# Kernel optimization log

Hardware: AMD Instinct MI355X
Metric: run time of the kernel (lower is better)

Reference implementation:

```python
import jax, jax.numpy as jnp
import numpy as np

TEMPERATURE = 1.0

def _rope_cos_sin(T, D):
    # inv_freq over even indices 0..D step 2 -> D//2 freqs
    inv_freq = 1.0 / (10000.0 ** (jnp.arange(0, D, 2, dtype=jnp.float32) / D))
    t = jnp.arange(T, dtype=jnp.float32)
    freqs = jnp.einsum('i,j->ij', t, inv_freq)          # [T, D//2]
    emb = jnp.concatenate([freqs, freqs], axis=-1)      # [T, D]
    return jnp.cos(emb), jnp.sin(emb)                   # each [T, D]

def _apply_rope(x, cos, sin):
    # x: [B,H,T,D]; cos/sin: [T,D] broadcast over B,H
    D = x.shape[-1]
    half = D // 2
    x1, x2 = x[..., :half], x[..., half:2 * half]
    c = cos[None, None, :, :half]
    s = sin[None, None, :, :half]
    rot = jnp.concatenate([x1 * c - x2 * s, x1 * s + x2 * c], axis=-1)
    if D > 2 * half:
        rot = jnp.concatenate([rot, x[..., 2 * half:]], axis=-1)
    return rot

def setup_inputs() -> dict:
    key = jax.random.key(0)
    kq, kk, kv = jax.random.split(key, 3)
    B, H, T, D = 2, 16, 2048, 64
    return {
        'q': jax.random.normal(kq, (B, H, T, D), dtype=jnp.float32),
        'k': jax.random.normal(kk, (B, H, T, D), dtype=jnp.float32),
        'v': jax.random.normal(kv, (B, H, T, D), dtype=jnp.float32),
    }

def reference(q, k, v):
    B, H, T, D = q.shape
    cos, sin = _rope_cos_sin(T, D)
    qr = _apply_rope(q, cos, sin)
    kr = _apply_rope(k, cos, sin)
    scale = jnp.sqrt(jnp.float32(D)) * TEMPERATURE
    scores = jnp.einsum('bhtd,bhsd->bhts', qr, kr) / scale  # [B,H,T,T]
    # original subtracts row max then softmax; identical to stable softmax
    attn = jax.nn.softmax(scores, axis=-1)
    out = jnp.einsum('bhts,bhsd->bhtd', attn, v)
    return out, attn
```

## Files before the change

kernel.cpp:

```cpp
#include <hip/hip_runtime.h>
#include <hip/hip_bf16.h>
#include <math.h>


#define T_SEQ  2048
#define D_HEAD 64
#define BH_N   32
#define NCH    32
#define OUT_ELEMS (BH_N * T_SEQ * D_HEAD)

typedef __attribute__((ext_vector_type(8))) short bf16x8;
typedef __attribute__((ext_vector_type(4))) float f32x4;

__device__ __forceinline__ unsigned short f2bf(float x) {
    __hip_bfloat16 h = __float2bfloat16(x);
    return *reinterpret_cast<unsigned short*>(&h);
}

__device__ __forceinline__ int swz(int o) { return o ^ (((o >> 7) & 7) << 4); }

__global__ void rope_table_kernel(float* __restrict__ ctab, float* __restrict__ stab) {
    int i = blockIdx.x * blockDim.x + threadIdx.x;
    if (i >= T_SEQ * 32) return;
    int t = i >> 5;
    int j = i & 31;
    float invf = powf(10000.0f, -(float)j / 32.0f);
    float a = (float)t * invf;
    ctab[i] = cosf(a);
    stab[i] = sinf(a);
}

__global__ __launch_bounds__(256)
void ropebf16_kernel(const float* __restrict__ X, const float* __restrict__ ctab,
                     const float* __restrict__ stab, unsigned short* __restrict__ H,
                     float scale)
{
    const int r  = blockIdx.x * 16 + (threadIdx.x >> 4);
    const int c4 = threadIdx.x & 15;
    const int t  = r & (T_SEQ - 1);
    const float4* xr = (const float4*)(X + (size_t)r * 64);
    float4 a = xr[c4];
    float4 b = xr[c4 ^ 8];
    float4 c = ((const float4*)(ctab + t * 32))[c4 & 7];
    float4 s = ((const float4*)(stab + t * 32))[c4 & 7];
    float4 ro;
    if (c4 < 8) {
        ro.x = a.x * c.x - b.x * s.x; ro.y = a.y * c.y - b.y * s.y;
        ro.z = a.z * c.z - b.z * s.z; ro.w = a.w * c.w - b.w * s.w;
    } else {
        ro.x = a.x * c.x + b.x * s.x; ro.y = a.y * c.y + b.y * s.y;
        ro.z = a.z * c.z + b.z * s.z; ro.w = a.w * c.w + b.w * s.w;
    }
    ushort4 h;
    h.x = f2bf(ro.x * scale); h.y = f2bf(ro.y * scale);
    h.z = f2bf(ro.z * scale); h.w = f2bf(ro.w * scale);
    *(ushort4*)(H + (size_t)r * 64 + c4 * 4) = h;
}

__global__ __launch_bounds__(256)
void vtbf16_kernel(const float* __restrict__ V, unsigned short* __restrict__ Vt)
{
    __shared__ float tile[64][65];
    const int bh = blockIdx.y;
    const int tt = blockIdx.x;
    const float* vg = V + ((size_t)bh * T_SEQ + tt * 64) * 64;
    #pragma unroll
    for (int i = 0; i < 4; ++i) {
        const int row = (threadIdx.x >> 4) + i * 16;
        const int c4  = threadIdx.x & 15;
        float4 a = *(const float4*)(vg + (size_t)row * 64 + c4 * 4);
        tile[row][c4 * 4 + 0] = a.x; tile[row][c4 * 4 + 1] = a.y;
        tile[row][c4 * 4 + 2] = a.z; tile[row][c4 * 4 + 3] = a.w;
    }
    __syncthreads();
    #pragma unroll
    for (int i = 0; i < 4; ++i) {
        const int d   = (threadIdx.x >> 4) + i * 16;
        const int tc4 = threadIdx.x & 15;
        ushort4 h;
        h.x = f2bf(tile[tc4 * 4 + 0][d]);
        h.y = f2bf(tile[tc4 * 4 + 1][d]);
        h.z = f2bf(tile[tc4 * 4 + 2][d]);
        h.w = f2bf(tile[tc4 * 4 + 3][d]);
        *(ushort4*)(Vt + ((size_t)bh * 64 + d) * T_SEQ + tt * 64 + tc4 * 4) = h;
    }
}

__global__ __launch_bounds__(256, 4)
void attn_mfma_kernel(const unsigned short* __restrict__ Qb,
                      const unsigned short* __restrict__ Kb,
                      const unsigned short* __restrict__ Vt,
                      float* __restrict__ out, float* __restrict__ attn)
{
    __shared__ __align__(16) unsigned short kbuf[3][64][64];
    __shared__ __align__(16) unsigned short pbuf[4][16][72];

    const int tid  = threadIdx.x;
    const int lane = tid & 63;
    const int w    = tid >> 6;
    const int lrow = lane & 15;
    const int lgrp = lane >> 4;

    const int lid = blockIdx.x;
    const int vid = (lid & 7) * 128 + (lid >> 3);
    const int bh  = vid >> 5;
    const int m   = vid & 31;
    const int t0  = m * 64 + w * 16;

    const size_t base = (size_t)bh * T_SEQ * D_HEAD;
    const char* kgb = (const char*)(Kb + base);
    const unsigned short* vgb = Vt + (size_t)bh * 64 * T_SEQ;

    bf16x8 qf0, qf1;
    {
        const unsigned short* qp = Qb + base + (size_t)(t0 + lrow) * 64 + lgrp * 8;
        qf0 = *(const bf16x8*)(qp);
        qf1 = *(const bf16x8*)(qp + 32);
    }

    const int so0 = w * 1024 + lane * 16;
    const int so1 = so0 + 4096;
    const int sq0 = swz(so0);
    const int sq1 = swz(so1);
    char* klds = (char*)&kbuf[0][0][0];
    char* plds = (char*)&pbuf[w][0][0];

#define STAGE_K(b, cc) do { \
    __builtin_amdgcn_global_load_lds((const unsigned int*)(kgb + (size_t)(cc) * 8192 + sq0), \
        (unsigned int*)(klds + (b) * 8192 + w * 1024), 16, 0, 0); \
    __builtin_amdgcn_global_load_lds((const unsigned int*)(kgb + (size_t)(cc) * 8192 + sq1), \
        (unsigned int*)(klds + (b) * 8192 + 4096 + w * 1024), 16, 0, 0); \
} while (0)

    float rpa0 = 0.f, rpa1 = 0.f, rpa2 = 0.f, rpa3 = 0.f;
    STAGE_K(0, 0);
    STAGE_K(1, 1);
    for (int cc = 0; cc < NCH; ++cc) {
        if (cc < NCH - 1) { asm volatile("s_waitcnt vmcnt(2)" ::: "memory"); }
        else              { asm volatile("s_waitcnt vmcnt(0)" ::: "memory"); }
        __builtin_amdgcn_s_barrier();
        if (cc + 2 < NCH) STAGE_K((cc + 2) % 3, cc + 2);
        __builtin_amdgcn_sched_barrier(0);
        const char* kb = klds + (cc % 3) * 8192;
        #pragma unroll
        for (int nt = 0; nt < 4; ++nt) {
            const int o = (nt * 16 + lrow) * 128 + lgrp * 16;
            bf16x8 a0 = *(const bf16x8*)(kb + swz(o));
            bf16x8 a1 = *(const bf16x8*)(kb + swz(o + 64));
            f32x4 acc = (f32x4){0.f, 0.f, 0.f, 0.f};
            acc = __builtin_amdgcn_mfma_f32_16x16x32_bf16(a0, qf0, acc, 0, 0, 0);
            acc = __builtin_amdgcn_mfma_f32_16x16x32_bf16(a1, qf1, acc, 0, 0, 0);
            rpa0 += __builtin_amdgcn_exp2f(acc[0]);
            rpa1 += __builtin_amdgcn_exp2f(acc[1]);
            rpa2 += __builtin_amdgcn_exp2f(acc[2]);
            rpa3 += __builtin_amdgcn_exp2f(acc[3]);
        }
    }
    float rp = (rpa0 + rpa1) + (rpa2 + rpa3);
    rp += __shfl_xor(rp, 16, 64);
    rp += __shfl_xor(rp, 32, 64);
    const float inv = 1.0f / rp;

    __builtin_amdgcn_sched_barrier(0);
    __builtin_amdgcn_s_barrier();

    f32x4 o4[4];
    #pragma unroll
    for (int nd = 0; nd < 4; ++nd) o4[nd] = (f32x4){0.f, 0.f, 0.f, 0.f};

    float* arow = attn + (size_t)bh * T_SEQ * T_SEQ + (size_t)(t0 + lrow) * T_SEQ + lgrp * 4;

    STAGE_K(0, 0);
    STAGE_K(1, 1);
    bf16x8 vf[8];
    #pragma unroll
    for (int nd = 0; nd < 4; ++nd)
        #pragma unroll
        for (int ks = 0; ks < 2; ++ks)
            vf[nd * 2 + ks] = *(const bf16x8*)(vgb + (size_t)(nd * 16 + lrow) * T_SEQ
                                               + ks * 32 + lgrp * 8);
    asm volatile("s_waitcnt vmcnt(10)" ::: "memory");

    for (int cc = 0; cc < NCH; ++cc) {
        __builtin_amdgcn_s_barrier();
        __builtin_amdgcn_sched_barrier(0);

        const char* kb = klds + (cc % 3) * 8192;
        f32x4 s4[4];
        #pragma unroll
        for (int nt = 0; nt < 4; ++nt) {
            const int o = (nt * 16 + lrow) * 128 + lgrp * 16;
            bf16x8 a0 = *(const bf16x8*)(kb + swz(o));
            bf16x8 a1 = *(const bf16x8*)(kb + swz(o + 64));
            f32x4 acc = (f32x4){0.f, 0.f, 0.f, 0.f};
            acc = __builtin_amdgcn_mfma_f32_16x16x32_bf16(a0, qf0, acc, 0, 0, 0);
            acc = __builtin_amdgcn_mfma_f32_16x16x32_bf16(a1, qf1, acc, 0, 0, 0);
            s4[nt] = acc;
        }
        #pragma unroll
        for (int nt = 0; nt < 4; ++nt) {
            s4[nt][0] = __builtin_amdgcn_exp2f(s4[nt][0]) * inv;
            s4[nt][1] = __builtin_amdgcn_exp2f(s4[nt][1]) * inv;
            s4[nt][2] = __builtin_amdgcn_exp2f(s4[nt][2]) * inv;
            s4[nt][3] = __builtin_amdgcn_exp2f(s4[nt][3]) * inv;
        }
        #pragma unroll
        for (int nt = 0; nt < 4; ++nt) {
            ushort4 p4;
            p4.x = f2bf(s4[nt][0]); p4.y = f2bf(s4[nt][1]);
            p4.z = f2bf(s4[nt][2]); p4.w = f2bf(s4[nt][3]);
            *(ushort4*)(plds + lrow * 144 + nt * 32 + lgrp * 8) = p4;
        }
        asm volatile("s_waitcnt lgkmcnt(0)" ::: "memory");
        __builtin_amdgcn_sched_barrier(0);
        #pragma unroll
        for (int ks = 0; ks < 2; ++ks) {
            bf16x8 pa = *(const bf16x8*)(plds + lrow * 144 + ks * 64 + lgrp * 16);
            #pragma unroll
            for (int nd = 0; nd < 4; ++nd)
                o4[nd] = __builtin_amdgcn_mfma_f32_16x16x32_bf16(pa, vf[nd * 2 + ks], o4[nd], 0, 0, 0);
        }
        __builtin_amdgcn_sched_barrier(0);
        if (cc + 1 < NCH) {
            #pragma unroll
            for (int nd = 0; nd < 4; ++nd)
                #pragma unroll
                for (int ks = 0; ks < 2; ++ks)
                    vf[nd * 2 + ks] = *(const bf16x8*)(vgb + (size_t)(nd * 16 + lrow) * T_SEQ
                                                       + (cc + 1) * 64 + ks * 32 + lgrp * 8);
        }
        if (cc + 2 < NCH) STAGE_K((cc + 2) % 3, cc + 2);
        __builtin_amdgcn_sched_barrier(0);
        #pragma unroll
        for (int nt = 0; nt < 4; ++nt)
            __builtin_nontemporal_store(s4[nt], (f32x4*)(arow + cc * 64 + nt * 16));
        __builtin_amdgcn_sched_barrier(0);
        if (cc < NCH - 2)      { asm volatile("s_waitcnt vmcnt(18)" ::: "memory"); }
        else if (cc < NCH - 1) { asm volatile("s_waitcnt vmcnt(16)" ::: "memory"); }
    }

    #pragma unroll
    for (int nd = 0; nd < 4; ++nd)
        #pragma unroll
        for (int j = 0; j < 4; ++j)
            __builtin_nontemporal_store(o4[nd][j],
                out + base + (size_t)(t0 + lgrp * 4 + j) * D_HEAD + nd * 16 + lrow);

#undef STAGE_K
}

extern "C" void kernel_launch(void* const* d_in, const int* in_sizes, int n_in,
                              void* d_out, int out_size, void* d_ws, size_t ws_size,
                              hipStream_t stream) {
    const float* q = (const float*)d_in[0];
    const float* k = (const float*)d_in[1];
    const float* v = (const float*)d_in[2];
    float* out  = (float*)d_out;
    float* attn = out + (size_t)OUT_ELEMS;

    float* ctab = (float*)d_ws;
    float* stab = ctab + T_SEQ * 32;
    unsigned short* wsu = (unsigned short*)(stab + T_SEQ * 32);
    const size_t NE = (size_t)BH_N * T_SEQ * D_HEAD;
    unsigned short* Qb = wsu + 0 * NE;
    unsigned short* Kb = wsu + 1 * NE;
    unsigned short* Vt = wsu + 2 * NE;

    const float QSCALE = 0.18033688011112042f;

    rope_table_kernel<<<dim3((T_SEQ * 32 + 255) / 256), dim3(256), 0, stream>>>(ctab, stab);
    ropebf16_kernel<<<dim3(BH_N * T_SEQ / 16), dim3(256), 0, stream>>>(q, ctab, stab, Qb, QSCALE);
    ropebf16_kernel<<<dim3(BH_N * T_SEQ / 16), dim3(256), 0, stream>>>(k, ctab, stab, Kb, 1.0f);
    vtbf16_kernel<<<dim3(T_SEQ / 64, BH_N), dim3(256), 0, stream>>>(v, Vt);
    attn_mfma_kernel<<<dim3(BH_N * T_SEQ / 64), dim3(256), 0, stream>>>(Qb, Kb, Vt, out, attn);
}
```

Baseline: 206.8 us.

## Stage fp32 probabilities in LDS for coalesced attn stores; merge Q/K rope launches

Softmax probabilities are now written to a swizzled per-wave fp32 LDS tile instead of a bf16 buffer. The tile is read back both as the bf16 MFMA operand (converted after the read) and transposed so each lane stores 16 contiguous bytes along the attention row. The goal is that each store instruction covers four full 256-byte row segments instead of scattered 16-byte pieces across 16 rows, which should make the dominant attn matrix write better coalesced. Separately, the Q and K rope kernels are merged into one launch using blockIdx.y, saving a launch. In exchange there is more LDS traffic and capacity (16 KB instead of about 9 KB), extra reads, and conversion work on the critical path.

New measurement: 183.5 us, median of 3. 1.13x faster.

```diff
diff --git a/kernel.cpp b/kernel.cpp
--- a/kernel.cpp
+++ b/kernel.cpp
@@ -18,6 +18,9 @@
 }
 
 __device__ __forceinline__ int swz(int o) { return o ^ (((o >> 7) & 7) << 4); }
+__device__ __forceinline__ int tswz(int row, int bcol) {
+    return row * 256 + (bcol ^ ((row & 7) << 4));
+}
 
 __global__ void rope_table_kernel(float* __restrict__ ctab, float* __restrict__ stab) {
     int i = blockIdx.x * blockDim.x + threadIdx.x;
@@ -31,13 +34,17 @@
 }
 
 __global__ __launch_bounds__(256)
-void ropebf16_kernel(const float* __restrict__ X, const float* __restrict__ ctab,
-                     const float* __restrict__ stab, unsigned short* __restrict__ H,
-                     float scale)
+void ropebf16_kernel(const float* __restrict__ Q, const float* __restrict__ K,
+                     const float* __restrict__ ctab, const float* __restrict__ stab,
+                     unsigned short* __restrict__ Qb, unsigned short* __restrict__ Kb,
+                     float qscale)
 {
     const int r  = blockIdx.x * 16 + (threadIdx.x >> 4);
     const int c4 = threadIdx.x & 15;
     const int t  = r & (T_SEQ - 1);
+    const float* X = blockIdx.y ? K : Q;
+    unsigned short* H = blockIdx.y ? Kb : Qb;
+    const float scale = blockIdx.y ? 1.0f : qscale;
     const float4* xr = (const float4*)(X + (size_t)r * 64);
     float4 a = xr[c4];
     float4 b = xr[c4 ^ 8];
@@ -93,7 +100,7 @@
                       float* __restrict__ out, float* __restrict__ attn)
 {
     __shared__ __align__(16) unsigned short kbuf[3][64][64];
-    __shared__ __align__(16) unsigned short pbuf[4][16][72];
+    __shared__ __align__(16) float tbuf[4][16 * 64];
 
     const int tid  = threadIdx.x;
     const int lane = tid & 63;
@@ -123,7 +130,7 @@
     const int sq0 = swz(so0);
     const int sq1 = swz(so1);
     char* klds = (char*)&kbuf[0][0][0];
-    char* plds = (char*)&pbuf[w][0][0];
+    char* tlds = (char*)&tbuf[w][0];
 
 #define STAGE_K(b, cc) do { \
     __builtin_amdgcn_global_load_lds((const unsigned int*)(kgb + (size_t)(cc) * 8192 + sq0), \
@@ -168,7 +175,7 @@
     #pragma unroll
     for (int nd = 0; nd < 4; ++nd) o4[nd] = (f32x4){0.f, 0.f, 0.f, 0.f};
 
-    float* arow = attn + (size_t)bh * T_SEQ * T_SEQ + (size_t)(t0 + lrow) * T_SEQ + lgrp * 4;
+    float* abase = attn + (size_t)bh * T_SEQ * T_SEQ;
 
     STAGE_K(0, 0);
     STAGE_K(1, 1);
@@ -205,21 +212,28 @@
             s4[nt][3] = __builtin_amdgcn_exp2f(s4[nt][3]) * inv;
         }
         #pragma unroll
-        for (int nt = 0; nt < 4; ++nt) {
-            ushort4 p4;
-            p4.x = f2bf(s4[nt][0]); p4.y = f2bf(s4[nt][1]);
-            p4.z = f2bf(s4[nt][2]); p4.w = f2bf(s4[nt][3]);
-            *(ushort4*)(plds + lrow * 144 + nt * 32 + lgrp * 8) = p4;
-        }
+        for (int nt = 0; nt < 4; ++nt)
+            *(f32x4*)(tlds + tswz(lrow, (nt * 16 + lgrp * 4) * 4)) = s4[nt];
         asm volatile("s_waitcnt lgkmcnt(0)" ::: "memory");
         __builtin_amdgcn_sched_barrier(0);
+
         #pragma unroll
         for (int ks = 0; ks < 2; ++ks) {
-            bf16x8 pa = *(const bf16x8*)(plds + lrow * 144 + ks * 64 + lgrp * 16);
+            f32x4 pa0 = *(const f32x4*)(tlds + tswz(lrow, (ks * 32 + lgrp * 8) * 4));
+            f32x4 pa1 = *(const f32x4*)(tlds + tswz(lrow, (ks * 32 + lgrp * 8 + 4) * 4));
+            bf16x8 pa;
+            pa[0] = (short)f2bf(pa0[0]); pa[1] = (short)f2bf(pa0[1]);
+            pa[2] = (short)f2bf(pa0[2]); pa[3] = (short)f2bf(pa0[3]);
+            pa[4] = (short)f2bf(pa1[0]); pa[5] = (short)f2bf(pa1[1]);
+            pa[6] = (short)f2bf(pa1[2]); pa[7] = (short)f2bf(pa1[3]);
             #pragma unroll
             for (int nd = 0; nd < 4; ++nd)
                 o4[nd] = __builtin_amdgcn_mfma_f32_16x16x32_bf16(pa, vf[nd * 2 + ks], o4[nd], 0, 0, 0);
         }
+        f32x4 tr[4];
+        #pragma unroll
+        for (int i = 0; i < 4; ++i)
+            tr[i] = *(const f32x4*)(tlds + tswz(i * 4 + (lane >> 4), (lane & 15) * 16));
         __builtin_amdgcn_sched_barrier(0);
         if (cc + 1 < NCH) {
             #pragma unroll
@@ -232,8 +246,10 @@
         if (cc + 2 < NCH) STAGE_K((cc + 2) % 3, cc + 2);
         __builtin_amdgcn_sched_barrier(0);
         #pragma unroll
-        for (int nt = 0; nt < 4; ++nt)
-            __builtin_nontemporal_store(s4[nt], (f32x4*)(arow + cc * 64 + nt * 16));
+        for (int i = 0; i < 4; ++i)
+            __builtin_nontemporal_store(tr[i],
+                (f32x4*)(abase + (size_t)(t0 + i * 4 + (lane >> 4)) * T_SEQ
+                         + cc * 64 + (lane & 15) * 4));
         __builtin_amdgcn_sched_barrier(0);
         if (cc < NCH - 2)      { asm volatile("s_waitcnt vmcnt(18)" ::: "memory"); }
         else if (cc < NCH - 1) { asm volatile("s_waitcnt vmcnt(16)" ::: "memory"); }
@@ -269,8 +285,7 @@
     const float QSCALE = 0.18033688011112042f;
 
     rope_table_kernel<<<dim3((T_SEQ * 32 + 255) / 256), dim3(256), 0, stream>>>(ctab, stab);
-    ropebf16_kernel<<<dim3(BH_N * T_SEQ / 16), dim3(256), 0, stream>>>(q, ctab, stab, Qb, QSCALE);
-    ropebf16_kernel<<<dim3(BH_N * T_SEQ / 16), dim3(256), 0, stream>>>(k, ctab, stab, Kb, 1.0f);
+    ropebf16_kernel<<<dim3(BH_N * T_SEQ / 16, 2), dim3(256), 0, stream>>>(q, k, ctab, stab, Qb, Kb, QSCALE);
     vtbf16_kernel<<<dim3(T_SEQ / 64, BH_N), dim3(256), 0, stream>>>(v, Vt);
     attn_mfma_kernel<<<dim3(BH_N * T_SEQ / 64), dim3(256), 0, stream>>>(Qb, Kb, Vt, out, attn);
 }
```
